# Kernel tuning notes

Hardware: AMD Instinct MI355X
Metric: run time of the kernel (lower is better)

The kernel has to match this reference:

```python
import jax, jax.numpy as jnp
import numpy as np

NUM_HEADS = 12
D = 768
HD = D // NUM_HEADS  # 64

def setup_inputs() -> dict:
    key = jax.random.key(0)
    ks = jax.random.split(key, 9)
    s = 0.02
    return {
        "x": jax.random.normal(ks[0], (4, 2048, D), dtype=jnp.float32),
        "QW_w": jax.random.normal(ks[1], (D, D), dtype=jnp.float32) * s,
        "QW_b": jax.random.normal(ks[2], (D,), dtype=jnp.float32) * s,
        "KW_w": jax.random.normal(ks[3], (D, D), dtype=jnp.float32) * s,
        "KW_b": jax.random.normal(ks[4], (D,), dtype=jnp.float32) * s,
        "VW_w": jax.random.normal(ks[5], (D, D), dtype=jnp.float32) * s,
        "VW_b": jax.random.normal(ks[6], (D,), dtype=jnp.float32) * s,
        "OW_w": jax.random.normal(ks[7], (D, D), dtype=jnp.float32) * s,
        "OW_b": jax.random.normal(ks[8], (D,), dtype=jnp.float32) * s,
    }

def reference(x, QW_w, QW_b, KW_w, KW_b, VW_w, VW_b, OW_w, OW_b):
    b, s, _ = x.shape
    # torch nn.Linear: y = x @ W.T + b
    def proj(w, bias):
        y = jnp.einsum('bsd,ed->bse', x, w) + bias
        return y.reshape(b, s, NUM_HEADS, HD).transpose(0, 2, 1, 3)  # [b,h,s,hd]
    q = proj(QW_w, QW_b)
    k = proj(KW_w, KW_b)
    v = proj(VW_w, VW_b)
    scores = jnp.einsum('bhqd,bhkd->bhqk', q, k) / jnp.sqrt(jnp.float32(HD))
    attn = jax.nn.softmax(scores, axis=-1)
    out = jnp.einsum('bhqk,bhkd->bhqd', attn, v)
    out = out.transpose(0, 2, 1, 3).reshape(b, s, NUM_HEADS * HD)
    return jnp.einsum('bsd,ed->bse', out, OW_w) + OW_b
```

## Files before the change

### kernel.cpp

```cpp
#include <hip/hip_runtime.h>
#include <hip/hip_bf16.h>

#define NH  12
#define HD  64
#define DIM 768
#define SEQ 2048
#define NB  4
#define MM  (NB*SEQ)
#define NKB (SEQ/64)

typedef short    v8s  __attribute__((ext_vector_type(8)));
typedef float    v4f  __attribute__((ext_vector_type(4)));
typedef float    v16f __attribute__((ext_vector_type(16)));
typedef unsigned v4u  __attribute__((ext_vector_type(4)));

#if __has_builtin(__builtin_amdgcn_exp2f)
#define EXP2(x) __builtin_amdgcn_exp2f(x)
#else
#define EXP2(x) __builtin_exp2f(x)
#endif

static __device__ __forceinline__ unsigned short f2b(float f) {
    unsigned int u = __float_as_uint(f);
    return (unsigned short)((u + 0x7FFFu + ((u >> 16) & 1u)) >> 16);
}
static __device__ __forceinline__ unsigned cvtpk(float lo, float hi) {
    unsigned r;
    asm("v_cvt_pk_bf16_f32 %0, %1, %2" : "=v"(r) : "v"(lo), "v"(hi));
    return r;
}
static __device__ __forceinline__ void g2l16(const unsigned short* g, unsigned short* l) {
    __builtin_amdgcn_global_load_lds(
        (const __attribute__((address_space(1))) void*)g,
        (__attribute__((address_space(3))) void*)l, 16, 0, 0);
}

__global__ void cast_f32_bf16(const float* __restrict__ in,
                              unsigned short* __restrict__ out, int n4) {
    int i = blockIdx.x * blockDim.x + threadIdx.x;
    if (i < n4) {
        float4 v = reinterpret_cast<const float4*>(in)[i];
        ushort4 o;
        o.x = f2b(v.x); o.y = f2b(v.y); o.z = f2b(v.z); o.w = f2b(v.w);
        reinterpret_cast<ushort4*>(out)[i] = o;
    }
}

__global__ void cast4_f32_bf16(const float* __restrict__ i0, const float* __restrict__ i1,
                               const float* __restrict__ i2, const float* __restrict__ i3,
                               unsigned short* __restrict__ o0, unsigned short* __restrict__ o1,
                               unsigned short* __restrict__ o2, unsigned short* __restrict__ o3,
                               int n4) {
    int i = blockIdx.x * blockDim.x + threadIdx.x;
    if (i >= n4) return;
    const float* in; unsigned short* out;
    switch (blockIdx.y) {
        case 0: in = i0; out = o0; break;
        case 1: in = i1; out = o1; break;
        case 2: in = i2; out = o2; break;
        default: in = i3; out = o3; break;
    }
    float4 v = reinterpret_cast<const float4*>(in)[i];
    ushort4 o;
    o.x = f2b(v.x); o.y = f2b(v.y); o.z = f2b(v.z); o.w = f2b(v.w);
    reinterpret_cast<ushort4*>(out)[i] = o;
}

__global__ __launch_bounds__(256, 3) void gemm_qkv(
    const unsigned short* __restrict__ A,
    const unsigned short* __restrict__ Wq,
    const unsigned short* __restrict__ Wk,
    const unsigned short* __restrict__ Wv,
    const float* __restrict__ bq,
    const float* __restrict__ bk,
    const float* __restrict__ bvp,
    unsigned short* __restrict__ Qb,
    unsigned short* __restrict__ Kfo,
    unsigned short* __restrict__ Vf)
{
    __shared__ __align__(16) unsigned short As[128 * 64];
    __shared__ __align__(16) unsigned short Bs[3][64 * 64];

    const int tid  = threadIdx.x;
    const int w    = tid >> 6, lane = tid & 63;
    const int quad = lane >> 4, l16 = lane & 15;
    const int wm   = w & 1,  wn = w >> 1;
    const int lane8 = lane >> 3, sc = lane & 7;
    const int m0   = blockIdx.x * 128;
    const int h    = blockIdx.y;
    const int n0   = h * 64;

    v4f acc[3][4][2];
    #pragma unroll
    for (int s = 0; s < 3; ++s)
        #pragma unroll
        for (int i = 0; i < 4; ++i)
            #pragma unroll
            for (int j = 0; j < 2; ++j)
                acc[s][i][j] = v4f{0.f, 0.f, 0.f, 0.f};

    for (int kb = 0; kb < DIM; kb += 64) {
        __syncthreads();
        #pragma unroll
        for (int t = 0; t < 4; ++t) {
            int r8 = w * 32 + t * 8;
            int r  = r8 + lane8;
            int gch = sc ^ (r & 7);
            g2l16(&A[(size_t)(m0 + r) * DIM + kb + gch * 8], &As[r8 * 64]);
        }
        #pragma unroll
        for (int u = 0; u < 6; ++u) {
            int G = w * 6 + u;
            int set = G >> 3, rg = G & 7;
            int row = rg * 8 + lane8;
            int gch = sc ^ (row & 7);
            const unsigned short* Wp = (set == 0) ? Wq : (set == 1) ? Wk : Wv;
            g2l16(&Wp[(size_t)(n0 + row) * DIM + kb + gch * 8], &Bs[set][rg * 8 * 64]);
        }
        __syncthreads();
        #pragma unroll
        for (int kk = 0; kk < 64; kk += 32) {
            int chb = kk >> 3;
            v8s a[4];
            #pragma unroll
            for (int i = 0; i < 4; ++i) {
                int m = wm * 64 + i * 16 + l16;
                a[i] = *reinterpret_cast<const v8s*>(
                    &As[m * 64 + (((chb + quad) ^ (m & 7)) << 3)]);
            }
            #pragma unroll
            for (int s = 0; s < 3; ++s) {
                v8s b[2];
                #pragma unroll
                for (int j = 0; j < 2; ++j) {
                    int n = wn * 32 + j * 16 + l16;
                    b[j] = *reinterpret_cast<const v8s*>(
                        &Bs[s][n * 64 + (((chb + quad) ^ (n & 7)) << 3)]);
                }
                #pragma unroll
                for (int i = 0; i < 4; ++i)
                    #pragma unroll
                    for (int j = 0; j < 2; ++j)
                        acc[s][i][j] = __builtin_amdgcn_mfma_f32_16x16x32_bf16(
                            a[i], b[j], acc[s][i][j], 0, 0, 0);
            }
        }
    }

    #pragma unroll
    for (int i = 0; i < 4; ++i) {
        #pragma unroll
        for (int j = 0; j < 2; ++j) {
            int hd = wn * 32 + j * 16 + l16;
            float bias_v = bq[n0 + hd];
            #pragma unroll
            for (int r = 0; r < 4; ++r) {
                int gm = m0 + wm * 64 + i * 16 + quad * 4 + r;
                int bb = gm >> 11, sq = gm & (SEQ - 1);
                Qb[((size_t)(bb * NH + h) * SEQ + sq) * HD + hd] =
                    f2b((acc[0][i][j][r] + bias_v) * 0.1803368801f);
            }
        }
    }
    #pragma unroll
    for (int i = 0; i < 4; ++i) {
        int kh = i >> 1;
        #pragma unroll
        for (int j = 0; j < 2; ++j) {
            int hd = wn * 32 + j * 16 + l16;
            int c  = hd >> 4;
            int half_a = (l16 >> 3) & 1;
            int jj = l16 & 7;
            float bias_v = bk[n0 + hd];
            int gm0 = m0 + wm * 64 + i * 16 + quad * 4;
            int bb = gm0 >> 11, sk = gm0 & (SEQ - 1);
            int t = sk >> 6;
            int l31k = (i & 1) * 16 + quad * 4;
            size_t frag = ((size_t)(bb * NH + h) * NKB + t) * 8 + kh * 4 + c;
            unsigned short* dst = &Kfo[frag * 512 + (half_a * 32 + l31k) * 8 + jj];
            #pragma unroll
            for (int r = 0; r < 4; ++r)
                dst[r * 8] = f2b(acc[1][i][j][r] + bias_v);
        }
    }
    #pragma unroll
    for (int i = 0; i < 4; ++i) {
        #pragma unroll
        for (int j = 0; j < 2; ++j) {
            int hd = wn * 32 + j * 16 + l16;
            int hb = hd >> 5, l31v = hd & 31;
            float bias_v = bvp[n0 + hd];
            int gm0 = m0 + wm * 64 + i * 16 + quad * 4;
            int bb = gm0 >> 11, sk = gm0 & (SEQ - 1);
            int kbi = sk >> 6;
            int halfv = quad >> 1, j0 = (quad & 1) * 4;
            ushort4 pkv;
            pkv.x = f2b(acc[2][i][j][0] + bias_v);
            pkv.y = f2b(acc[2][i][j][1] + bias_v);
            pkv.z = f2b(acc[2][i][j][2] + bias_v);
            pkv.w = f2b(acc[2][i][j][3] + bias_v);
            size_t frag = ((size_t)(bb * NH + h) * NKB + kbi) * 8 + hb * 4 + i;
            *reinterpret_cast<ushort4*>(
                &Vf[frag * 512 + (halfv * 32 + l31v) * 8 + j0]) = pkv;
        }
    }
}

__global__ __launch_bounds__(256, 3) void gemm_o(
    const unsigned short* __restrict__ A,
    const unsigned short* __restrict__ W,
    const float* __restrict__ bias,
    float* __restrict__ out)
{
    __shared__ __align__(16) unsigned short As[128 * 64];
    __shared__ __align__(16) unsigned short Bs[64 * 64];

    const int tid  = threadIdx.x;
    const int w    = tid >> 6, lane = tid & 63;
    const int quad = lane >> 4, l16 = lane & 15;
    const int wm   = w & 1,  wn = w >> 1;
    const int lane8 = lane >> 3, sc = lane & 7;
    const int m0  = blockIdx.x * 128;
    const int n0l = blockIdx.y * 64;

    v4f acc[4][2];
    #pragma unroll
    for (int i = 0; i < 4; ++i)
        #pragma unroll
        for (int j = 0; j < 2; ++j)
            acc[i][j] = v4f{0.f, 0.f, 0.f, 0.f};

    for (int kb = 0; kb < DIM; kb += 64) {
        __syncthreads();
        #pragma unroll
        for (int t = 0; t < 4; ++t) {
            int r8 = w * 32 + t * 8;
            int r  = r8 + lane8;
            int gch = sc ^ (r & 7);
            g2l16(&A[(size_t)(m0 + r) * DIM + kb + gch * 8], &As[r8 * 64]);
        }
        #pragma unroll
        for (int t = 0; t < 2; ++t) {
            int r8 = (w * 2 + t) * 8;
            int r  = r8 + lane8;
            int gch = sc ^ (r & 7);
            g2l16(&W[(size_t)(n0l + r) * DIM + kb + gch * 8], &Bs[r8 * 64]);
        }
        __syncthreads();
        #pragma unroll
        for (int kk = 0; kk < 64; kk += 32) {
            v8s a[4], b[2];
            int chb = kk >> 3;
            #pragma unroll
            for (int i = 0; i < 4; ++i) {
                int m = wm * 64 + i * 16 + l16;
                a[i] = *reinterpret_cast<const v8s*>(
                    &As[m * 64 + (((chb + quad) ^ (m & 7)) << 3)]);
            }
            #pragma unroll
            for (int j = 0; j < 2; ++j) {
                int n = wn * 32 + j * 16 + l16;
                b[j] = *reinterpret_cast<const v8s*>(
                    &Bs[n * 64 + (((chb + quad) ^ (n & 7)) << 3)]);
            }
            #pragma unroll
            for (int i = 0; i < 4; ++i)
                #pragma unroll
                for (int j = 0; j < 2; ++j)
                    acc[i][j] = __builtin_amdgcn_mfma_f32_16x16x32_bf16(a[i], b[j], acc[i][j], 0, 0, 0);
        }
    }

    #pragma unroll
    for (int i = 0; i < 4; ++i) {
        #pragma unroll
        for (int j = 0; j < 2; ++j) {
            int gn = n0l + wn * 32 + j * 16 + l16;
            float bias_v = bias[gn];
            #pragma unroll
            for (int r = 0; r < 4; ++r) {
                int gm = m0 + wm * 64 + i * 16 + quad * 4 + r;
                out[(size_t)gm * DIM + gn] = acc[i][j][r] + bias_v;
            }
        }
    }
}

__global__ __launch_bounds__(256, 3) void attn(
    const unsigned short* __restrict__ Q,
    const unsigned short* __restrict__ Kf,
    const unsigned short* __restrict__ Vf,
    unsigned short* __restrict__ ctx)
{
    const int tid  = threadIdx.x;
    const int w    = tid >> 6, lane = tid & 63;
    const int l31  = lane & 31, half = lane >> 5;
    const int bh   = blockIdx.y;
    const int b    = bh / NH, h = bh % NH;
    const int q0   = blockIdx.x * 128 + w * 32;

    const unsigned short* Qp = Q  + ((size_t)bh * SEQ + q0) * HD;
    const unsigned short* Vh = Vf + (size_t)bh * (NKB * 8 * 512) + lane * 8;
    const unsigned short* Kh = Kf + (size_t)bh * (NKB * 8 * 512) + lane * 8;

    v8s bq[4];
    #pragma unroll
    for (int c = 0; c < 4; ++c)
        bq[c] = *reinterpret_cast<const v8s*>(&Qp[l31 * HD + c * 16 + half * 8]);

    v8s ka[2][4], va[2][4];
    #pragma unroll
    for (int g = 0; g < 8; ++g)
        reinterpret_cast<v8s*>(ka)[g] = *reinterpret_cast<const v8s*>(&Kh[g * 512]);
    #pragma unroll
    for (int g = 0; g < 8; ++g)
        reinterpret_cast<v8s*>(va)[g] = *reinterpret_cast<const v8s*>(&Vh[g * 512]);

    v16f o0, o1, Z;
    #pragma unroll
    for (int i = 0; i < 16; ++i) { o0[i] = 0.f; o1[i] = 0.f; Z[i] = 0.f; }
    float li = 0.f;

    for (int it = 0; it < NKB; ++it) {
        v16f s0 = __builtin_amdgcn_mfma_f32_32x32x16_bf16(ka[0][0], bq[0], Z, 0, 0, 0);
        v16f s1 = __builtin_amdgcn_mfma_f32_32x32x16_bf16(ka[1][0], bq[0], Z, 0, 0, 0);
        #pragma unroll
        for (int c = 1; c < 4; ++c) {
            s0 = __builtin_amdgcn_mfma_f32_32x32x16_bf16(ka[0][c], bq[c], s0, 0, 0, 0);
            s1 = __builtin_amdgcn_mfma_f32_32x32x16_bf16(ka[1][c], bq[c], s1, 0, 0, 0);
        }

        {
            const unsigned short* Kn = Kh + (size_t)(it + 1 < NKB ? it + 1 : it) * (8 * 512);
            #pragma unroll
            for (int g = 0; g < 8; ++g)
                reinterpret_cast<v8s*>(ka)[g] = *reinterpret_cast<const v8s*>(&Kn[g * 512]);
        }

        unsigned pk[8][2];
        #pragma unroll
        for (int g = 0; g < 4; ++g) {
            float e0 = EXP2(s0[4*g+0]), e1 = EXP2(s0[4*g+1]);
            float e2 = EXP2(s0[4*g+2]), e3 = EXP2(s0[4*g+3]);
            li += (e0 + e1) + (e2 + e3);
            pk[g][0] = cvtpk(e0, e1);
            pk[g][1] = cvtpk(e2, e3);
            float f0 = EXP2(s1[4*g+0]), f1 = EXP2(s1[4*g+1]);
            float f2 = EXP2(s1[4*g+2]), f3 = EXP2(s1[4*g+3]);
            li += (f0 + f1) + (f2 + f3);
            pk[4+g][0] = cvtpk(f0, f1);
            pk[4+g][1] = cvtpk(f2, f3);
        }

        #pragma unroll
        for (int cp = 0; cp < 4; ++cp) {
            unsigned a0 = pk[2*cp][0],   a1 = pk[2*cp][1];
            unsigned b0 = pk[2*cp+1][0], b1 = pk[2*cp+1][1];
            unsigned u0 = half ? a0 : b0;
            unsigned u1 = half ? a1 : b1;
            unsigned x0 = __shfl_xor(u0, 32);
            unsigned x1 = __shfl_xor(u1, 32);
            v4u fw;
            fw.x = half ? x0 : a0;
            fw.y = half ? x1 : a1;
            fw.z = half ? b0 : x0;
            fw.w = half ? b1 : x1;
            v8s pf = __builtin_bit_cast(v8s, fw);
            o0 = __builtin_amdgcn_mfma_f32_32x32x16_bf16(va[0][cp], pf, o0, 0, 0, 0);
            o1 = __builtin_amdgcn_mfma_f32_32x32x16_bf16(va[1][cp], pf, o1, 0, 0, 0);
        }

        {
            const unsigned short* Vn = Vh + (size_t)(it + 1 < NKB ? it + 1 : it) * (8 * 512);
            #pragma unroll
            for (int g = 0; g < 8; ++g)
                reinterpret_cast<v8s*>(va)[g] = *reinterpret_cast<const v8s*>(&Vn[g * 512]);
        }
    }

    float inv = 1.0f / (li + __shfl_xor(li, 32));

    const int q = q0 + l31;
    size_t base = ((size_t)(b * SEQ + q)) * DIM + h * HD;
    #pragma unroll
    for (int g = 0; g < 4; ++g) {
        int hd0 = 8 * g + 4 * half;
        uint2 u0, u1;
        u0.x = cvtpk(o0[4*g+0] * inv, o0[4*g+1] * inv);
        u0.y = cvtpk(o0[4*g+2] * inv, o0[4*g+3] * inv);
        u1.x = cvtpk(o1[4*g+0] * inv, o1[4*g+1] * inv);
        u1.y = cvtpk(o1[4*g+2] * inv, o1[4*g+3] * inv);
        *reinterpret_cast<uint2*>(&ctx[base + hd0])      = u0;
        *reinterpret_cast<uint2*>(&ctx[base + 32 + hd0]) = u1;
    }
}

extern "C" void kernel_launch(void* const* d_in, const int* in_sizes, int n_in,
                              void* d_out, int out_size, void* d_ws, size_t ws_size,
                              hipStream_t stream) {
    const float* x  = (const float*)d_in[0];
    const float* qw = (const float*)d_in[1]; const float* qb = (const float*)d_in[2];
    const float* kw = (const float*)d_in[3]; const float* kb = (const float*)d_in[4];
    const float* vw = (const float*)d_in[5]; const float* vb = (const float*)d_in[6];
    const float* ow = (const float*)d_in[7]; const float* ob = (const float*)d_in[8];
    float* out = (float*)d_out;

    char* ws = (char*)d_ws;
    size_t off = 0;
    auto alloc = [&](size_t bytes) -> unsigned short* {
        unsigned short* p = (unsigned short*)(ws + off);
        off += (bytes + 255) & ~(size_t)255;
        return p;
    };
    const size_t XB = (size_t)MM * DIM * 2;
    const size_t WB = (size_t)DIM * DIM * 2;
    const size_t QB = (size_t)NB * NH * SEQ * HD * 2;

    unsigned short* xb  = alloc(XB);
    unsigned short* wqb = alloc(WB);
    unsigned short* wkb = alloc(WB);
    unsigned short* wvb = alloc(WB);
    unsigned short* wob = alloc(WB);
    unsigned short* Qb  = alloc(QB);
    unsigned short* Kfb = alloc(QB);
    unsigned short* Vfb = alloc(QB);
    unsigned short* ctx = alloc(XB);

    const int n4x = MM * DIM / 4;
    const int n4w = DIM * DIM / 4;
    cast_f32_bf16<<<(n4x + 255) / 256, 256, 0, stream>>>(x, xb, n4x);
    cast4_f32_bf16<<<dim3((n4w + 255) / 256, 4), 256, 0, stream>>>(
        qw, kw, vw, ow, wqb, wkb, wvb, wob, n4w);

    gemm_qkv<<<dim3(MM / 128, NH), 256, 0, stream>>>(
        xb, wqb, wkb, wvb, qb, kb, vb, Qb, Kfb, Vfb);

    attn<<<dim3(SEQ / 128, NB * NH), 256, 0, stream>>>(Qb, Kfb, Vfb, ctx);

    gemm_o<<<dim3(MM / 128, DIM / 64), 256, 0, stream>>>(ctx, wob, ob, out);
}
```

Measured before the change: 241.5 us.

## Stage K tiles in double-buffered LDS shared across waves; prefetch V two tiles ahead

K tiles are now loaded cooperatively into a double-buffered LDS buffer with direct global-to-LDS copies, each wave fetching two of the eight chunks, instead of every wave loading the full K tile into registers. V is kept in registers with two alternating buffers prefetched two iterations ahead. Block indices are also remapped so that blocks working on the same head run close together. This cuts redundant global K traffic and register pressure at the cost of a block-wide barrier and a vmcnt wait each iteration.

```diff
diff --git a/kernel.cpp b/kernel.cpp
--- a/kernel.cpp
+++ b/kernel.cpp
@@ -286,96 +286,137 @@
     }
 }
 
+static __device__ __forceinline__ void tile_step(
+    int it, int buf,
+    const unsigned short* __restrict__ Kh,
+    const unsigned short* __restrict__ Vh,
+    unsigned short (&Ks)[2][8 * 512],
+    int w, int lane, int half,
+    const v8s (&bq)[4], v8s (&VA)[2][4],
+    v16f& o0, v16f& o1, const v16f& Z, float& li)
+{
+    asm volatile("s_waitcnt vmcnt(8)" ::: "memory");
+    __builtin_amdgcn_s_barrier();
+    __builtin_amdgcn_sched_barrier(0);
+
+    {
+        int nt = (it + 1 < NKB) ? it + 1 : it;
+        #pragma unroll
+        for (int t = 0; t < 2; ++t) {
+            int g = w * 2 + t;
+            g2l16(&Kh[((size_t)nt * 8 + g) * 512 + lane * 8], &Ks[buf ^ 1][g * 512]);
+        }
+    }
+    __builtin_amdgcn_sched_barrier(0);
+
+    const unsigned short* Kb_ = Ks[buf];
+    v16f s0, s1;
+    {
+        v8s k0 = *reinterpret_cast<const v8s*>(&Kb_[lane * 8]);
+        v8s k1 = *reinterpret_cast<const v8s*>(&Kb_[4 * 512 + lane * 8]);
+        s0 = __builtin_amdgcn_mfma_f32_32x32x16_bf16(k0, bq[0], Z, 0, 0, 0);
+        s1 = __builtin_amdgcn_mfma_f32_32x32x16_bf16(k1, bq[0], Z, 0, 0, 0);
+        #pragma unroll
+        for (int c = 1; c < 4; ++c) {
+            v8s kc0 = *reinterpret_cast<const v8s*>(&Kb_[(size_t)c * 512 + lane * 8]);
+            v8s kc1 = *reinterpret_cast<const v8s*>(&Kb_[(size_t)(4 + c) * 512 + lane * 8]);
+            s0 = __builtin_amdgcn_mfma_f32_32x32x16_bf16(kc0, bq[c], s0, 0, 0, 0);
+            s1 = __builtin_amdgcn_mfma_f32_32x32x16_bf16(kc1, bq[c], s1, 0, 0, 0);
+        }
+    }
+
+    unsigned pk[8][2];
+    #pragma unroll
+    for (int g = 0; g < 4; ++g) {
+        float e0 = EXP2(s0[4*g+0]), e1 = EXP2(s0[4*g+1]);
+        float e2 = EXP2(s0[4*g+2]), e3 = EXP2(s0[4*g+3]);
+        li += (e0 + e1) + (e2 + e3);
+        pk[g][0] = cvtpk(e0, e1);
+        pk[g][1] = cvtpk(e2, e3);
+        float f0 = EXP2(s1[4*g+0]), f1 = EXP2(s1[4*g+1]);
+        float f2 = EXP2(s1[4*g+2]), f3 = EXP2(s1[4*g+3]);
+        li += (f0 + f1) + (f2 + f3);
+        pk[4+g][0] = cvtpk(f0, f1);
+        pk[4+g][1] = cvtpk(f2, f3);
+    }
+
+    #pragma unroll
+    for (int cp = 0; cp < 4; ++cp) {
+        unsigned a0 = pk[2*cp][0],   a1 = pk[2*cp][1];
+        unsigned b0 = pk[2*cp+1][0], b1 = pk[2*cp+1][1];
+        unsigned u0 = half ? a0 : b0;
+        unsigned u1 = half ? a1 : b1;
+        unsigned x0 = __shfl_xor(u0, 32);
+        unsigned x1 = __shfl_xor(u1, 32);
+        v4u fw;
+        fw.x = half ? x0 : a0;
+        fw.y = half ? x1 : a1;
+        fw.z = half ? b0 : x0;
+        fw.w = half ? b1 : x1;
+        v8s pf = __builtin_bit_cast(v8s, fw);
+        o0 = __builtin_amdgcn_mfma_f32_32x32x16_bf16(VA[0][cp], pf, o0, 0, 0, 0);
+        o1 = __builtin_amdgcn_mfma_f32_32x32x16_bf16(VA[1][cp], pf, o1, 0, 0, 0);
+    }
+
+    {
+        int ntv = (it + 2 < NKB) ? it + 2 : it;
+        #pragma unroll
+        for (int g = 0; g < 8; ++g)
+            reinterpret_cast<v8s*>(VA)[g] =
+                *reinterpret_cast<const v8s*>(&Vh[((size_t)ntv * 8 + g) * 512]);
+    }
+}
+
 __global__ __launch_bounds__(256, 3) void attn(
     const unsigned short* __restrict__ Q,
     const unsigned short* __restrict__ Kf,
     const unsigned short* __restrict__ Vf,
     unsigned short* __restrict__ ctx)
 {
+    __shared__ __align__(16) unsigned short Ks[2][8 * 512];
+
     const int tid  = threadIdx.x;
     const int w    = tid >> 6, lane = tid & 63;
     const int l31  = lane & 31, half = lane >> 5;
-    const int bh   = blockIdx.y;
+
+    const int lblk = blockIdx.y * 16 + blockIdx.x;
+    const int vblk = (lblk & 7) * 96 + (lblk >> 3);
+    const int bh   = vblk >> 4;
     const int b    = bh / NH, h = bh % NH;
-    const int q0   = blockIdx.x * 128 + w * 32;
+    const int q0   = (vblk & 15) * 128 + w * 32;
 
     const unsigned short* Qp = Q  + ((size_t)bh * SEQ + q0) * HD;
     const unsigned short* Vh = Vf + (size_t)bh * (NKB * 8 * 512) + lane * 8;
-    const unsigned short* Kh = Kf + (size_t)bh * (NKB * 8 * 512) + lane * 8;
+    const unsigned short* Kh = Kf + (size_t)bh * (NKB * 8 * 512);
 
     v8s bq[4];
     #pragma unroll
     for (int c = 0; c < 4; ++c)
         bq[c] = *reinterpret_cast<const v8s*>(&Qp[l31 * HD + c * 16 + half * 8]);
 
-    v8s ka[2][4], va[2][4];
+    #pragma unroll
+    for (int t = 0; t < 2; ++t) {
+        int g = w * 2 + t;
+        g2l16(&Kh[(size_t)g * 512 + lane * 8], &Ks[0][g * 512]);
+    }
+    __builtin_amdgcn_sched_barrier(0);
+
+    v8s vaA[2][4], vaB[2][4];
     #pragma unroll
     for (int g = 0; g < 8; ++g)
-        reinterpret_cast<v8s*>(ka)[g] = *reinterpret_cast<const v8s*>(&Kh[g * 512]);
+        reinterpret_cast<v8s*>(vaA)[g] = *reinterpret_cast<const v8s*>(&Vh[(size_t)g * 512]);
     #pragma unroll
     for (int g = 0; g < 8; ++g)
-        reinterpret_cast<v8s*>(va)[g] = *reinterpret_cast<const v8s*>(&Vh[g * 512]);
+        reinterpret_cast<v8s*>(vaB)[g] = *reinterpret_cast<const v8s*>(&Vh[(size_t)(8 + g) * 512]);
 
     v16f o0, o1, Z;
     #pragma unroll
     for (int i = 0; i < 16; ++i) { o0[i] = 0.f; o1[i] = 0.f; Z[i] = 0.f; }
     float li = 0.f;
 
-    for (int it = 0; it < NKB; ++it) {
-        v16f s0 = __builtin_amdgcn_mfma_f32_32x32x16_bf16(ka[0][0], bq[0], Z, 0, 0, 0);
-        v16f s1 = __builtin_amdgcn_mfma_f32_32x32x16_bf16(ka[1][0], bq[0], Z, 0, 0, 0);
-        #pragma unroll
-        for (int c = 1; c < 4; ++c) {
-            s0 = __builtin_amdgcn_mfma_f32_32x32x16_bf16(ka[0][c], bq[c], s0, 0, 0, 0);
-            s1 = __builtin_amdgcn_mfma_f32_32x32x16_bf16(ka[1][c], bq[c], s1, 0, 0, 0);
-        }
-
-        {
-            const unsigned short* Kn = Kh + (size_t)(it + 1 < NKB ? it + 1 : it) * (8 * 512);
-            #pragma unroll
-            for (int g = 0; g < 8; ++g)
-                reinterpret_cast<v8s*>(ka)[g] = *reinterpret_cast<const v8s*>(&Kn[g * 512]);
-        }
-
-        unsigned pk[8][2];
-        #pragma unroll
-        for (int g = 0; g < 4; ++g) {
-            float e0 = EXP2(s0[4*g+0]), e1 = EXP2(s0[4*g+1]);
-            float e2 = EXP2(s0[4*g+2]), e3 = EXP2(s0[4*g+3]);
-            li += (e0 + e1) + (e2 + e3);
-            pk[g][0] = cvtpk(e0, e1);
-            pk[g][1] = cvtpk(e2, e3);
-            float f0 = EXP2(s1[4*g+0]), f1 = EXP2(s1[4*g+1]);
-            float f2 = EXP2(s1[4*g+2]), f3 = EXP2(s1[4*g+3]);
-            li += (f0 + f1) + (f2 + f3);
-            pk[4+g][0] = cvtpk(f0, f1);
-            pk[4+g][1] = cvtpk(f2, f3);
-        }
-
-        #pragma unroll
-        for (int cp = 0; cp < 4; ++cp) {
-            unsigned a0 = pk[2*cp][0],   a1 = pk[2*cp][1];
-            unsigned b0 = pk[2*cp+1][0], b1 = pk[2*cp+1][1];
-            unsigned u0 = half ? a0 : b0;
-            unsigned u1 = half ? a1 : b1;
-            unsigned x0 = __shfl_xor(u0, 32);
-            unsigned x1 = __shfl_xor(u1, 32);
-            v4u fw;
-            fw.x = half ? x0 : a0;
-            fw.y = half ? x1 : a1;
-            fw.z = half ? b0 : x0;
-            fw.w = half ? b1 : x1;
-            v8s pf = __builtin_bit_cast(v8s, fw);
-            o0 = __builtin_amdgcn_mfma_f32_32x32x16_bf16(va[0][cp], pf, o0, 0, 0, 0);
-            o1 = __builtin_amdgcn_mfma_f32_32x32x16_bf16(va[1][cp], pf, o1, 0, 0, 0);
-        }
-
-        {
-            const unsigned short* Vn = Vh + (size_t)(it + 1 < NKB ? it + 1 : it) * (8 * 512);
-            #pragma unroll
-            for (int g = 0; g < 8; ++g)
-                reinterpret_cast<v8s*>(va)[g] = *reinterpret_cast<const v8s*>(&Vn[g * 512]);
-        }
+    for (int it = 0; it < NKB; it += 2) {
+        tile_step(it,     0, Kh, Vh, Ks, w, lane, half, bq, vaA, o0, o1, Z, li);
+        tile_step(it + 1, 1, Kh, Vh, Ks, w, lane, half, bq, vaB, o0, o1, Z, li);
     }
 
     float inv = 1.0f / (li + __shfl_xor(li, 32));
```

New measurement: 211.1 us. 1.14x faster.
